# Kernel optimization log

Hardware: AMD Instinct MI355X
Metric: run time of the kernel (lower is better)

Reference implementation:

```python
import jax, jax.numpy as jnp
import numpy as np

N = 50000      # nodes
E = 800000     # edges (avg degree 16)
F_IN = 128     # num_node_features
H = 128        # hidden_dim
G = 500        # num graphs in batch


def setup_inputs() -> dict:
    key = jax.random.key(0)
    ks = jax.random.split(key, 20)
    inp = {
        "x": jax.random.normal(ks[0], (N, F_IN), dtype=jnp.float32),
        "edge_index": jax.random.randint(ks[1], (2, E), 0, N, dtype=jnp.int32),
        "batch": jnp.sort(jax.random.randint(ks[2], (N,), 0, G, dtype=jnp.int32)),
    }
    s = 0.05
    # 3 GIN layers: MLP = Linear -> ReLU -> Linear, plus learnable eps (init 0)
    dims = [(F_IN, H), (H, H), (H, H)]
    for i, (din, dout) in enumerate(dims):
        k = jax.random.split(ks[3 + i], 4)
        inp[f"W1_{i}"] = jax.random.normal(k[0], (din, H), dtype=jnp.float32) * s
        inp[f"b1_{i}"] = jnp.zeros((H,), dtype=jnp.float32)
        inp[f"W2_{i}"] = jax.random.normal(k[1], (H, dout), dtype=jnp.float32) * s
        inp[f"b2_{i}"] = jnp.zeros((dout,), dtype=jnp.float32)
        inp[f"eps_{i}"] = jnp.zeros((), dtype=jnp.float32)
    inp["fc_w"] = jax.random.normal(ks[10], (H, 1), dtype=jnp.float32) * s
    inp["fc_b"] = jnp.zeros((1,), dtype=jnp.float32)
    return inp


def _gin_layer(x, src, dst, eps, W1, b1, W2, b2):
    # neighbor sum: scatter-add messages x[src] into dst rows
    agg = jax.ops.segment_sum(x[src], dst, num_segments=N)  # [N, d]
    h = (1.0 + eps) * x + agg
    h = jax.nn.relu(h @ W1 + b1) @ W2 + b2
    return h


def reference(x, edge_index, batch,
              W1_0, b1_0, W2_0, b2_0, eps_0,
              W1_1, b1_1, W2_1, b2_1, eps_1,
              W1_2, b1_2, W2_2, b2_2, eps_2,
              fc_w, fc_b):
    src, dst = edge_index[0], edge_index[1]
    layers = [(eps_0, W1_0, b1_0, W2_0, b2_0),
              (eps_1, W1_1, b1_1, W2_1, b2_1),
              (eps_2, W1_2, b1_2, W2_2, b2_2)]
    h = x
    for i, (eps, W1, b1, W2, b2) in enumerate(layers):
        h = _gin_layer(h, src, dst, eps, W1, b1, W2, b2)
        if i < len(layers) - 1:
            h = jax.nn.relu(h)  # dropout is identity in eval mode
    # global mean pool over graph ids
    sums = jax.ops.segment_sum(h, batch, num_segments=G)          # [G, H]
    counts = jax.ops.segment_sum(jnp.ones((N,), h.dtype), batch, num_segments=G)
    pooled = sums / jnp.maximum(counts, 1.0)[:, None]
    out = pooled @ fc_w + fc_b  # [G, 1]
    return jnp.squeeze(out, axis=-1)  # [G]
```

## Files before the change

kernel.cpp:

```cpp
#include <hip/hip_runtime.h>


#define FEAT 128
#define BCAP 2048
#define CHUNK 10240

typedef short  bf16x8 __attribute__((ext_vector_type(8)));
typedef float  f32x4  __attribute__((ext_vector_type(4)));

__device__ inline unsigned short f2bf(float f) {
    unsigned int u = __float_as_uint(f);
    u = (u + 0x7FFFu + ((u >> 16) & 1u)) >> 16;
    return (unsigned short)u;
}
__device__ inline float2 bfpair(unsigned int u) {
    float2 r;
    r.x = __uint_as_float(u << 16);
    r.y = __uint_as_float(u & 0xffff0000u);
    return r;
}

__global__ __launch_bounds__(1024) void bucket_kernel(
    const int* __restrict__ src, const int* __restrict__ dst,
    int* __restrict__ bcnt, unsigned int* __restrict__ bpairs, int E) {
    __shared__ unsigned int lpairs[CHUNK];
    __shared__ int lbase[1025];
    __shared__ int lcur[1024];
    __shared__ int lres[1024];
    __shared__ int part[1024];
    int tid = threadIdx.x;
    int e0 = blockIdx.x * CHUNK;
    int e1 = e0 + CHUNK; if (e1 > E) e1 = E;
    int cnt = e1 - e0;
    lcur[tid] = 0;
    __syncthreads();
    for (int e = e0 + tid; e < e1; e += 1024) atomicAdd(&lcur[dst[e] >> 6], 1);
    __syncthreads();
    int v = lcur[tid];
    part[tid] = v;
    __syncthreads();
    for (int d = 1; d < 1024; d <<= 1) {
        int u = (tid >= d) ? part[tid - d] : 0;
        __syncthreads();
        part[tid] += u;
        __syncthreads();
    }
    int ex = part[tid] - v;
    lbase[tid] = ex;
    if (tid == 1023) lbase[1024] = part[1023];
    lcur[tid] = ex;
    lres[tid] = (v > 0) ? atomicAdd(&bcnt[tid * 16], v) : 0;
    __syncthreads();
    for (int e = e0 + tid; e < e1; e += 1024) {
        int d = dst[e], s = src[e];
        int p = atomicAdd(&lcur[d >> 6], 1);
        lpairs[p] = ((unsigned int)s << 6) | (unsigned int)(d & 63);
    }
    __syncthreads();
    for (int j = tid; j < cnt; j += 1024) {
        int lo = 0, hi = 1023;
        while (lo < hi) { int m = (lo + hi + 1) >> 1; if (lbase[m] <= j) lo = m; else hi = m - 1; }
        int gpos = lres[lo] + (j - lbase[lo]);
        if (gpos < BCAP) bpairs[(size_t)lo * BCAP + gpos] = lpairs[j];
    }
}

__global__ void scan_bcnt_kernel(const int* __restrict__ bcnt, int* __restrict__ bbase,
                                 int* __restrict__ off, int n, int nbuckets) {
    __shared__ int l[1024];
    int t = threadIdx.x;
    int v = (t < nbuckets) ? bcnt[t * 16] : 0;
    l[t] = v;
    __syncthreads();
    for (int d = 1; d < 1024; d <<= 1) {
        int u = (t >= d) ? l[t - d] : 0;
        __syncthreads();
        l[t] += u;
        __syncthreads();
    }
    if (t < nbuckets) bbase[t] = l[t] - v;
    if (t == 1023) off[n] = l[1023];
}

__global__ __launch_bounds__(256) void degscat_kernel(
    const int* __restrict__ bcnt, const int* __restrict__ bbase,
    const unsigned int* __restrict__ bpairs,
    int* __restrict__ off, int* __restrict__ srcs, int n) {
    __shared__ int lh[64];
    __shared__ int lcur[64];
    int b = blockIdx.x, tid = threadIdx.x;
    if (tid < 64) lh[tid] = 0;
    __syncthreads();
    int cnt = bcnt[b * 16]; if (cnt > BCAP) cnt = BCAP;
    int base = bbase[b];
    const unsigned int* bp = bpairs + (size_t)b * BCAP;
    for (int i = tid; i < cnt; i += 256) atomicAdd(&lh[bp[i] & 63u], 1);
    __syncthreads();
    if (tid < 64) {
        int v = lh[tid];
        int inc = v;
        #pragma unroll
        for (int d = 1; d < 64; d <<= 1) {
            int u = __shfl_up(inc, d, 64);
            if (tid >= d) inc += u;
        }
        int ex = base + inc - v;
        int node = b * 64 + tid;
        if (node < n) off[node] = ex;
        lcur[tid] = ex;
    }
    __syncthreads();
    for (int i = tid; i < cnt; i += 256) {
        unsigned int pr = bp[i];
        int pos = atomicAdd(&lcur[pr & 63u], 1);
        srcs[pos] = (int)(pr >> 6);
    }
}

__global__ __launch_bounds__(256) void setup_kernel(
    const float* __restrict__ x, unsigned int* __restrict__ xbf, long pairs, int nxb,
    const int* __restrict__ batch, int* __restrict__ gstart, int n, int G,
    const float* __restrict__ W2f, const float* __restrict__ b2f,
    const float* __restrict__ fcw, float* __restrict__ weff,
    const float* __restrict__ W0, const float* __restrict__ W1,
    const float* __restrict__ W2, const float* __restrict__ W3,
    const float* __restrict__ W4, unsigned short* __restrict__ Wswz) {
    int b = blockIdx.x, tid = threadIdx.x;
    if (b < nxb) {
        long i = (long)b * 256 + tid;
        if (i < pairs) {
            float2 v = ((const float2*)x)[i];
            unsigned int pk = (unsigned int)f2bf(v.x) | ((unsigned int)f2bf(v.y) << 16);
            long node = i >> 6;
            int dg = (int)(i & 63);
            int slice = dg >> 4, d = dg & 15;
            xbf[(size_t)slice * n * 16 + node * 16 + d] = pk;
        }
    } else if (b < nxb + 2) {
        int i = (b - nxb) * 256 + tid;
        if (i <= G) {
            int lo = 0, hi = n;
            while (lo < hi) { int m = (lo + hi) >> 1; if (batch[m] < i) lo = m + 1; else hi = m; }
            gstart[i] = lo;
        }
    } else if (b == nxb + 2) {
        int lane = tid & 63, wave = tid >> 6;
        float2 f2 = ((const float2*)fcw)[lane];
        for (int r = wave; r < 128; r += 4) {
            float2 w = ((const float2*)(W2f + r * FEAT))[lane];
            float d = w.x * f2.x + w.y * f2.y;
            #pragma unroll
            for (int s = 32; s; s >>= 1) d += __shfl_down(d, s, 64);
            if (lane == 0) weff[r] = d;
        }
        if (wave == 0) {
            float2 bb = ((const float2*)b2f)[lane];
            float d = bb.x * f2.x + bb.y * f2.y;
            #pragma unroll
            for (int s = 32; s; s >>= 1) d += __shfl_down(d, s, 64);
            if (lane == 0) weff[128] = d;
        }
    } else {
        int gid = (b - nxb - 3) * 256 + tid;
        if (gid < 5 * 2048) {
            int mat = gid >> 11;
            int task = gid & 2047;
            int c = task >> 4, m = task & 15;
            const float* W = (mat == 0) ? W0 : (mat == 1) ? W1 : (mat == 2) ? W2 :
                             (mat == 3) ? W3 : W4;
            unsigned short* dp = Wswz + mat * 16384 + c * 128 + ((m ^ (c & 7)) << 3);
            #pragma unroll
            for (int j = 0; j < 8; ++j) dp[j] = f2bf(W[(8 * m + j) * FEAT + c]);
        }
    }
}

__global__ __launch_bounds__(256) void agg_kernel(
    const unsigned int* __restrict__ hs, const int* __restrict__ off,
    const int* __restrict__ srcs, const float* __restrict__ eps_p,
    unsigned int* __restrict__ pre, int n) {
    int b = blockIdx.x;
    int slice = b & 3;
    int chunk = b >> 2;
    int tid = threadIdx.x;
    int wave = tid >> 6, lane = tid & 63;
    int g = lane >> 2, d = lane & 3;
    int node = chunk * 64 + wave * 16 + g;
    if (node >= n) return;
    float eps1 = 1.0f + eps_p[0];
    const uint4* hb = (const uint4*)(hs + (size_t)slice * n * 16);
    uint4 su = hb[(size_t)node * 4 + d];
    float2 p0 = bfpair(su.x), p1 = bfpair(su.y), p2 = bfpair(su.z), p3 = bfpair(su.w);
    float4 a0 = make_float4(p0.x * eps1, p0.y * eps1, p1.x * eps1, p1.y * eps1);
    float4 b0 = make_float4(p2.x * eps1, p2.y * eps1, p3.x * eps1, p3.y * eps1);
    float4 a1 = make_float4(0.f, 0.f, 0.f, 0.f), b1v = a1;
    float4 a2 = a1, b2v = a1;
    float4 a3 = a1, b3v = a1;
    int j0 = off[node], j1 = off[node + 1];
    int j = j0;
    #define ACC(A, B, U) { float2 q0 = bfpair(U.x), q1 = bfpair(U.y), \
                                  q2 = bfpair(U.z), q3 = bfpair(U.w); \
        A.x += q0.x; A.y += q0.y; A.z += q1.x; A.w += q1.y; \
        B.x += q2.x; B.y += q2.y; B.z += q3.x; B.w += q3.y; }
    for (; j + 8 <= j1; j += 8) {
        int s0 = srcs[j], s1 = srcs[j + 1], s2 = srcs[j + 2], s3 = srcs[j + 3];
        int s4 = srcs[j + 4], s5 = srcs[j + 5], s6 = srcs[j + 6], s7 = srcs[j + 7];
        uint4 u0 = hb[(size_t)s0 * 4 + d];
        uint4 u1 = hb[(size_t)s1 * 4 + d];
        uint4 u2 = hb[(size_t)s2 * 4 + d];
        uint4 u3 = hb[(size_t)s3 * 4 + d];
        uint4 u4 = hb[(size_t)s4 * 4 + d];
        uint4 u5 = hb[(size_t)s5 * 4 + d];
        uint4 u6 = hb[(size_t)s6 * 4 + d];
        uint4 u7 = hb[(size_t)s7 * 4 + d];
        ACC(a0, b0, u0) ACC(a1, b1v, u1) ACC(a2, b2v, u2) ACC(a3, b3v, u3)
        ACC(a0, b0, u4) ACC(a1, b1v, u5) ACC(a2, b2v, u6) ACC(a3, b3v, u7)
    }
    for (; j + 4 <= j1; j += 4) {
        int s0 = srcs[j], s1 = srcs[j + 1], s2 = srcs[j + 2], s3 = srcs[j + 3];
        uint4 u0 = hb[(size_t)s0 * 4 + d];
        uint4 u1 = hb[(size_t)s1 * 4 + d];
        uint4 u2 = hb[(size_t)s2 * 4 + d];
        uint4 u3 = hb[(size_t)s3 * 4 + d];
        ACC(a0, b0, u0) ACC(a1, b1v, u1) ACC(a2, b2v, u2) ACC(a3, b3v, u3)
    }
    for (; j < j1; ++j) {
        uint4 u = hb[(size_t)srcs[j] * 4 + d];
        ACC(a0, b0, u)
    }
    #undef ACC
    a0.x += a1.x + a2.x;  a0.y += a1.y + a2.y;
    a0.z += a1.z + a2.z;  a0.w += a1.w + a2.w;
    a0.x += a3.x;  a0.y += a3.y;  a0.z += a3.z;  a0.w += a3.w;
    b0.x += b1v.x + b2v.x;  b0.y += b1v.y + b2v.y;
    b0.z += b1v.z + b2v.z;  b0.w += b1v.w + b2v.w;
    b0.x += b3v.x;  b0.y += b3v.y;  b0.z += b3v.z;  b0.w += b3v.w;
    uint4 o;
    o.x = (unsigned int)f2bf(a0.x) | ((unsigned int)f2bf(a0.y) << 16);
    o.y = (unsigned int)f2bf(a0.z) | ((unsigned int)f2bf(a0.w) << 16);
    o.z = (unsigned int)f2bf(b0.x) | ((unsigned int)f2bf(b0.y) << 16);
    o.w = (unsigned int)f2bf(b0.z) | ((unsigned int)f2bf(b0.w) << 16);
    ((uint4*)(pre + (size_t)slice * n * 16))[(size_t)node * 4 + d] = o;
}

template <int MODE>
__global__ __launch_bounds__(256) void mfma_mlp_kernel(
    const unsigned short* __restrict__ A, const unsigned short* __restrict__ Wswz,
    const float* __restrict__ bias, unsigned short* __restrict__ outbf,
    const int* __restrict__ batch, const float* __restrict__ weff,
    float* __restrict__ sums, int n) {
    __shared__ int4 Wl4[2048];
    int tid = threadIdx.x;
    const int4* ws4 = (const int4*)Wswz;
    #pragma unroll
    for (int i = 0; i < 8; ++i) Wl4[i * 256 + tid] = ws4[i * 256 + tid];
    __syncthreads();
    const unsigned short* Wl = (const unsigned short*)Wl4;

    int lane = tid & 63, wave = tid >> 6;
    int q = lane >> 4, c15 = lane & 15;
    int r0 = blockIdx.x * 64 + wave * 16;
    int arow = r0 + c15;
    bool rv = arow < n;
    size_t sstride = (size_t)n * 32;
    const unsigned short* abase = A + (size_t)arow * 32 + 8 * q;

    f32x4 zf = {0.f, 0.f, 0.f, 0.f};
    f32x4 acc[8];
    #pragma unroll
    for (int i = 0; i < 8; ++i) acc[i] = zf;
    bf16x8 zero8 = {0, 0, 0, 0, 0, 0, 0, 0};

    #pragma unroll
    for (int k0 = 0; k0 < 4; ++k0) {
        bf16x8 a = rv ? *(const bf16x8*)(abase + (size_t)k0 * sstride) : zero8;
        int m = k0 * 4 + q;
        #pragma unroll
        for (int nt = 0; nt < 8; ++nt) {
            int col = nt * 16 + c15;
            bf16x8 bfr = *(const bf16x8*)&Wl[col * 128 + ((m ^ (col & 7)) << 3)];
            acc[nt] = __builtin_amdgcn_mfma_f32_16x16x32_bf16(a, bfr, acc[nt], 0, 0, 0);
        }
    }

    int orow0 = r0 + q * 4;
    if (MODE == 1) {
        #pragma unroll
        for (int nt = 0; nt < 8; ++nt) {
            float bv = bias[nt * 16 + c15];
            size_t sb = (size_t)(nt >> 1) * sstride + (nt & 1) * 16 + c15;
            #pragma unroll
            for (int r = 0; r < 4; ++r) {
                int ro = orow0 + r;
                if (ro < n) {
                    float v = fmaxf(acc[nt][r] + bv, 0.f);
                    outbf[sb + (size_t)ro * 32] = f2bf(v);
                }
            }
        }
    } else {
        __shared__ float gsum[64];
        int r0b = blockIdx.x * 64;
        int lastn = r0b + 63 < n - 1 ? r0b + 63 : n - 1;
        int gmin = batch[r0b];
        int gmax = batch[lastn];
        int span = gmax - gmin + 1;
        bool lds_ok = (span <= 64);
        if (lds_ok) for (int i = tid; i < span; i += 256) gsum[i] = 0.f;
        __syncthreads();
        float rowdot[4] = {0.f, 0.f, 0.f, 0.f};
        #pragma unroll
        for (int nt = 0; nt < 8; ++nt) {
            int col = nt * 16 + c15;
            float bv = bias[col];
            float wv = weff[col];
            #pragma unroll
            for (int r = 0; r < 4; ++r)
                rowdot[r] += fmaxf(acc[nt][r] + bv, 0.f) * wv;
        }
        #pragma unroll
        for (int r = 0; r < 4; ++r) {
            float v = rowdot[r];
            v += __shfl_xor(v, 1, 64);
            v += __shfl_xor(v, 2, 64);
            v += __shfl_xor(v, 4, 64);
            v += __shfl_xor(v, 8, 64);
            if (c15 == 0) {
                int node = orow0 + r;
                if (node < n) {
                    int g = batch[node];
                    if (lds_ok) atomicAdd(&gsum[g - gmin], v);
                    else        atomicAdd(&sums[g], v);
                }
            }
        }
        __syncthreads();
        if (lds_ok)
            for (int i = tid; i < span; i += 256) atomicAdd(&sums[gmin + i], gsum[i]);
    }
}

__global__ void finalize_kernel(const float* __restrict__ sums, const int* __restrict__ gstart,
                                const float* __restrict__ weff, const float* __restrict__ fcb,
                                float* __restrict__ out, int G) {
    int g = blockIdx.x * blockDim.x + threadIdx.x;
    if (g >= G) return;
    int cnt = gstart[g + 1] - gstart[g];
    out[g] = (cnt > 0) ? sums[g] / (float)cnt + weff[128] + fcb[0] : fcb[0];
}

static inline size_t align256(size_t x) { return (x + 255) & ~(size_t)255; }

extern "C" void kernel_launch(void* const* d_in, const int* in_sizes, int n_in,
                              void* d_out, int out_size, void* d_ws, size_t ws_size,
                              hipStream_t stream) {
    const float* x      = (const float*)d_in[0];
    const int*   ei     = (const int*)d_in[1];
    const int*   batch  = (const int*)d_in[2];
    const float* W1[3]  = {(const float*)d_in[3],  (const float*)d_in[8],  (const float*)d_in[13]};
    const float* b1[3]  = {(const float*)d_in[4],  (const float*)d_in[9],  (const float*)d_in[14]};
    const float* W2[3]  = {(const float*)d_in[5],  (const float*)d_in[10], (const float*)d_in[15]};
    const float* b2[3]  = {(const float*)d_in[6],  (const float*)d_in[11], (const float*)d_in[16]};
    const float* eps[3] = {(const float*)d_in[7],  (const float*)d_in[12], (const float*)d_in[17]};
    const float* fcw    = (const float*)d_in[18];
    const float* fcb    = (const float*)d_in[19];
    float* out = (float*)d_out;

    const int N = in_sizes[0] / FEAT;
    const int E = in_sizes[1] / 2;
    const int G = out_size;
    const int nbuckets = (N + 63) >> 6;

    char* p = (char*)d_ws;
    int* off    = (int*)p;  p += align256((size_t)(N + 1) * 4);
    int* srcs   = (int*)p;  p += align256((size_t)E * 4);
    int* bbase  = (int*)p;  p += align256((size_t)1024 * 4);
    int* gstart = (int*)p;  p += align256((size_t)(G + 1) * 4);
    float* weff = (float*)p; p += align256((size_t)256 * 4);
    unsigned short* Wswz = (unsigned short*)p; p += align256((size_t)5 * 16384 * 2);
    float* sums = (float*)p;
    char* z0 = (char*)sums;
    p += align256((size_t)G * 4);
    int* bcnt = (int*)p; p += align256((size_t)nbuckets * 16 * 4);
    size_t zbytes = (size_t)(p - z0);
    unsigned int* bpairs = (unsigned int*)p;     p += align256((size_t)nbuckets * BCAP * 4);
    unsigned int* x_bf   = (unsigned int*)p;     p += align256((size_t)N * 64 * 4);
    unsigned int* pre_bf = (unsigned int*)p;     p += align256((size_t)N * 64 * 4);
    unsigned int* t_bf   = (unsigned int*)p;     p += align256((size_t)N * 64 * 4);
    unsigned int* h_bf   = (unsigned int*)p;     p += align256((size_t)N * 64 * 4);
    (void)ws_size; (void)n_in;

    const int* src = ei;
    const int* dst = ei + E;

    hipMemsetAsync(z0, 0, zbytes, stream);

    const int nchunks = (E + CHUNK - 1) / CHUNK;
    bucket_kernel<<<nchunks, 1024, 0, stream>>>(src, dst, bcnt, bpairs, E);
    scan_bcnt_kernel<<<1, 1024, 0, stream>>>(bcnt, bbase, off, N, nbuckets);
    degscat_kernel<<<nbuckets, 256, 0, stream>>>(bcnt, bbase, bpairs, off, srcs, N);

    long pairs = (long)N * 64;
    int nxb = (int)((pairs + 255) / 256);
    setup_kernel<<<nxb + 43, 256, 0, stream>>>(
        x, x_bf, pairs, nxb, batch, gstart, N, G,
        W2[2], b2[2], fcw, weff,
        W1[0], W2[0], W1[1], W2[1], W1[2], Wswz);

    const int aggBlocks  = 4 * ((N + 63) / 64);
    const int gemmBlocks = (N + 63) / 64;
    const unsigned short* Wz[5] = {Wswz, Wswz + 16384, Wswz + 2 * 16384,
                                   Wswz + 3 * 16384, Wswz + 4 * 16384};

    const unsigned int* h = x_bf;
    for (int i = 0; i < 2; ++i) {
        agg_kernel<<<aggBlocks, 256, 0, stream>>>(h, off, srcs, eps[i], pre_bf, N);
        mfma_mlp_kernel<1><<<gemmBlocks, 256, 0, stream>>>(
            (const unsigned short*)pre_bf, Wz[2 * i], b1[i], (unsigned short*)t_bf,
            nullptr, nullptr, nullptr, N);
        mfma_mlp_kernel<1><<<gemmBlocks, 256, 0, stream>>>(
            (const unsigned short*)t_bf, Wz[2 * i + 1], b2[i], (unsigned short*)h_bf,
            nullptr, nullptr, nullptr, N);
        h = h_bf;
    }
    agg_kernel<<<aggBlocks, 256, 0, stream>>>(h, off, srcs, eps[2], pre_bf, N);
    mfma_mlp_kernel<2><<<gemmBlocks, 256, 0, stream>>>(
        (const unsigned short*)pre_bf, Wz[4], b1[2], nullptr,
        batch, weff, sums, N);

    finalize_kernel<<<(G + 255) / 256, 256, 0, stream>>>(sums, gstart, weff, fcb, out, G);
}
```

Baseline: 295.5 us.

## Merge setup kernels, drop bucket scan kernel, fold finalize into last GEMM

Bucketing and the setup work (bf16 conversion, graph starts, weight swizzle, folded fc weights) now run as one 1024-thread launch. The separate bucket-count scan kernel is removed: each degscat block sums the preceding bucket counts itself, and off[n] is set to E directly. The finalize kernel is replaced by a last-block-done pattern inside the final MLP kernel, using an atomic counter and a thread fence. The aim is to cut three launches and their gaps, at the cost of redundant prefix sums in degscat, larger blocks for the conversion work, and off[n]=E being wrong if any bucket overflows BCAP.

```diff
diff --git a/kernel.cpp b/kernel.cpp
--- a/kernel.cpp
+++ b/kernel.cpp
@@ -20,114 +20,63 @@
     return r;
 }
 
-__global__ __launch_bounds__(1024) void bucket_kernel(
+__global__ __launch_bounds__(1024) void front_kernel(
     const int* __restrict__ src, const int* __restrict__ dst,
-    int* __restrict__ bcnt, unsigned int* __restrict__ bpairs, int E) {
-    __shared__ unsigned int lpairs[CHUNK];
-    __shared__ int lbase[1025];
-    __shared__ int lcur[1024];
-    __shared__ int lres[1024];
-    __shared__ int part[1024];
-    int tid = threadIdx.x;
-    int e0 = blockIdx.x * CHUNK;
-    int e1 = e0 + CHUNK; if (e1 > E) e1 = E;
-    int cnt = e1 - e0;
-    lcur[tid] = 0;
-    __syncthreads();
-    for (int e = e0 + tid; e < e1; e += 1024) atomicAdd(&lcur[dst[e] >> 6], 1);
-    __syncthreads();
-    int v = lcur[tid];
-    part[tid] = v;
-    __syncthreads();
-    for (int d = 1; d < 1024; d <<= 1) {
-        int u = (tid >= d) ? part[tid - d] : 0;
-        __syncthreads();
-        part[tid] += u;
-        __syncthreads();
-    }
-    int ex = part[tid] - v;
-    lbase[tid] = ex;
-    if (tid == 1023) lbase[1024] = part[1023];
-    lcur[tid] = ex;
-    lres[tid] = (v > 0) ? atomicAdd(&bcnt[tid * 16], v) : 0;
-    __syncthreads();
-    for (int e = e0 + tid; e < e1; e += 1024) {
-        int d = dst[e], s = src[e];
-        int p = atomicAdd(&lcur[d >> 6], 1);
-        lpairs[p] = ((unsigned int)s << 6) | (unsigned int)(d & 63);
-    }
-    __syncthreads();
-    for (int j = tid; j < cnt; j += 1024) {
-        int lo = 0, hi = 1023;
-        while (lo < hi) { int m = (lo + hi + 1) >> 1; if (lbase[m] <= j) lo = m; else hi = m - 1; }
-        int gpos = lres[lo] + (j - lbase[lo]);
-        if (gpos < BCAP) bpairs[(size_t)lo * BCAP + gpos] = lpairs[j];
-    }
-}
-
-__global__ void scan_bcnt_kernel(const int* __restrict__ bcnt, int* __restrict__ bbase,
-                                 int* __restrict__ off, int n, int nbuckets) {
-    __shared__ int l[1024];
-    int t = threadIdx.x;
-    int v = (t < nbuckets) ? bcnt[t * 16] : 0;
-    l[t] = v;
-    __syncthreads();
-    for (int d = 1; d < 1024; d <<= 1) {
-        int u = (t >= d) ? l[t - d] : 0;
-        __syncthreads();
-        l[t] += u;
-        __syncthreads();
-    }
-    if (t < nbuckets) bbase[t] = l[t] - v;
-    if (t == 1023) off[n] = l[1023];
-}
-
-__global__ __launch_bounds__(256) void degscat_kernel(
-    const int* __restrict__ bcnt, const int* __restrict__ bbase,
-    const unsigned int* __restrict__ bpairs,
-    int* __restrict__ off, int* __restrict__ srcs, int n) {
-    __shared__ int lh[64];
-    __shared__ int lcur[64];
-    int b = blockIdx.x, tid = threadIdx.x;
-    if (tid < 64) lh[tid] = 0;
-    __syncthreads();
-    int cnt = bcnt[b * 16]; if (cnt > BCAP) cnt = BCAP;
-    int base = bbase[b];
-    const unsigned int* bp = bpairs + (size_t)b * BCAP;
-    for (int i = tid; i < cnt; i += 256) atomicAdd(&lh[bp[i] & 63u], 1);
-    __syncthreads();
-    if (tid < 64) {
-        int v = lh[tid];
-        int inc = v;
-        #pragma unroll
-        for (int d = 1; d < 64; d <<= 1) {
-            int u = __shfl_up(inc, d, 64);
-            if (tid >= d) inc += u;
-        }
-        int ex = base + inc - v;
-        int node = b * 64 + tid;
-        if (node < n) off[node] = ex;
-        lcur[tid] = ex;
-    }
-    __syncthreads();
-    for (int i = tid; i < cnt; i += 256) {
-        unsigned int pr = bp[i];
-        int pos = atomicAdd(&lcur[pr & 63u], 1);
-        srcs[pos] = (int)(pr >> 6);
-    }
-}
-
-__global__ __launch_bounds__(256) void setup_kernel(
-    const float* __restrict__ x, unsigned int* __restrict__ xbf, long pairs, int nxb,
+    int* __restrict__ bcnt, unsigned int* __restrict__ bpairs, int E, int nchunks,
+    const float* __restrict__ x, unsigned int* __restrict__ xbf, long pairs, int nxbf,
     const int* __restrict__ batch, int* __restrict__ gstart, int n, int G,
     const float* __restrict__ W2f, const float* __restrict__ b2f,
     const float* __restrict__ fcw, float* __restrict__ weff,
     const float* __restrict__ W0, const float* __restrict__ W1,
     const float* __restrict__ W2, const float* __restrict__ W3,
     const float* __restrict__ W4, unsigned short* __restrict__ Wswz) {
+    __shared__ unsigned int lpairs[CHUNK];
+    __shared__ int lbase[1025];
+    __shared__ int lcur[1024];
+    __shared__ int lres[1024];
+    __shared__ int part[1024];
     int b = blockIdx.x, tid = threadIdx.x;
-    if (b < nxb) {
-        long i = (long)b * 256 + tid;
+
+    if (b < nchunks) {
+        int e0 = b * CHUNK;
+        int e1 = e0 + CHUNK; if (e1 > E) e1 = E;
+        int cnt = e1 - e0;
+        lcur[tid] = 0;
+        __syncthreads();
+        for (int e = e0 + tid; e < e1; e += 1024) atomicAdd(&lcur[dst[e] >> 6], 1);
+        __syncthreads();
+        int v = lcur[tid];
+        part[tid] = v;
+        __syncthreads();
+        for (int d = 1; d < 1024; d <<= 1) {
+            int u = (tid >= d) ? part[tid - d] : 0;
+            __syncthreads();
+            part[tid] += u;
+            __syncthreads();
+        }
+        int ex = part[tid] - v;
+        lbase[tid] = ex;
+        if (tid == 1023) lbase[1024] = part[1023];
+        lcur[tid] = ex;
+        lres[tid] = (v > 0) ? atomicAdd(&bcnt[tid * 16], v) : 0;
+        __syncthreads();
+        for (int e = e0 + tid; e < e1; e += 1024) {
+            int d = dst[e], s = src[e];
+            int p = atomicAdd(&lcur[d >> 6], 1);
+            lpairs[p] = ((unsigned int)s << 6) | (unsigned int)(d & 63);
+        }
+        __syncthreads();
+        for (int j = tid; j < cnt; j += 1024) {
+            int lo = 0, hi = 1023;
+            while (lo < hi) { int m = (lo + hi + 1) >> 1; if (lbase[m] <= j) lo = m; else hi = m - 1; }
+            int gpos = lres[lo] + (j - lbase[lo]);
+            if (gpos < BCAP) bpairs[(size_t)lo * BCAP + gpos] = lpairs[j];
+        }
+        return;
+    }
+    b -= nchunks;
+    if (b < nxbf) {
+        long i = (long)b * 1024 + tid;
         if (i < pairs) {
             float2 v = ((const float2*)x)[i];
             unsigned int pk = (unsigned int)f2bf(v.x) | ((unsigned int)f2bf(v.y) << 16);
@@ -136,17 +85,21 @@
             int slice = dg >> 4, d = dg & 15;
             xbf[(size_t)slice * n * 16 + node * 16 + d] = pk;
         }
-    } else if (b < nxb + 2) {
-        int i = (b - nxb) * 256 + tid;
-        if (i <= G) {
+        return;
+    }
+    b -= nxbf;
+    if (b == 0) {
+        for (int i = tid; i <= G; i += 1024) {
             int lo = 0, hi = n;
             while (lo < hi) { int m = (lo + hi) >> 1; if (batch[m] < i) lo = m + 1; else hi = m; }
             gstart[i] = lo;
         }
-    } else if (b == nxb + 2) {
+        return;
+    }
+    if (b == 1) {
         int lane = tid & 63, wave = tid >> 6;
         float2 f2 = ((const float2*)fcw)[lane];
-        for (int r = wave; r < 128; r += 4) {
+        for (int r = wave; r < 128; r += 16) {
             float2 w = ((const float2*)(W2f + r * FEAT))[lane];
             float d = w.x * f2.x + w.y * f2.y;
             #pragma unroll
@@ -160,8 +113,10 @@
             for (int s = 32; s; s >>= 1) d += __shfl_down(d, s, 64);
             if (lane == 0) weff[128] = d;
         }
-    } else {
-        int gid = (b - nxb - 3) * 256 + tid;
+        return;
+    }
+    {
+        int gid = (b - 2) * 1024 + tid;
         if (gid < 5 * 2048) {
             int mat = gid >> 11;
             int task = gid & 2047;
@@ -172,6 +127,45 @@
             #pragma unroll
             for (int j = 0; j < 8; ++j) dp[j] = f2bf(W[(8 * m + j) * FEAT + c]);
         }
+    }
+}
+
+__global__ __launch_bounds__(256) void degscat_kernel(
+    const int* __restrict__ bcnt, const unsigned int* __restrict__ bpairs,
+    int* __restrict__ off, int* __restrict__ srcs, int n, int E) {
+    __shared__ int lh[64];
+    __shared__ int lcur[64];
+    int b = blockIdx.x, tid = threadIdx.x;
+    if (tid < 64) lh[tid] = 0;
+    if (b == 0 && tid == 0) off[n] = E;
+    __syncthreads();
+    int cnt = bcnt[b * 16]; if (cnt > BCAP) cnt = BCAP;
+    const unsigned int* bp = bpairs + (size_t)b * BCAP;
+    for (int i = tid; i < cnt; i += 256) atomicAdd(&lh[bp[i] & 63u], 1);
+    __syncthreads();
+    if (tid < 64) {
+        int bp_ = 0;
+        for (int k = tid; k < b; k += 64) bp_ += bcnt[k * 16];
+        #pragma unroll
+        for (int d = 32; d; d >>= 1) bp_ += __shfl_down(bp_, d, 64);
+        int base = __shfl(bp_, 0, 64);
+        int v = lh[tid];
+        int inc = v;
+        #pragma unroll
+        for (int d = 1; d < 64; d <<= 1) {
+            int u = __shfl_up(inc, d, 64);
+            if (tid >= d) inc += u;
+        }
+        int ex = base + inc - v;
+        int node = b * 64 + tid;
+        if (node < n) off[node] = ex;
+        lcur[tid] = ex;
+    }
+    __syncthreads();
+    for (int i = tid; i < cnt; i += 256) {
+        unsigned int pr = bp[i];
+        int pos = atomicAdd(&lcur[pr & 63u], 1);
+        srcs[pos] = (int)(pr >> 6);
     }
 }
 
@@ -248,7 +242,9 @@
     const unsigned short* __restrict__ A, const unsigned short* __restrict__ Wswz,
     const float* __restrict__ bias, unsigned short* __restrict__ outbf,
     const int* __restrict__ batch, const float* __restrict__ weff,
-    float* __restrict__ sums, int n) {
+    float* __restrict__ sums, int* __restrict__ donecnt,
+    const int* __restrict__ gstart, const float* __restrict__ fcb,
+    float* __restrict__ out, int G, int n) {
     __shared__ int4 Wl4[2048];
     int tid = threadIdx.x;
     const int4* ws4 = (const int4*)Wswz;
@@ -300,6 +296,7 @@
         }
     } else {
         __shared__ float gsum[64];
+        __shared__ int amlast;
         int r0b = blockIdx.x * 64;
         int lastn = r0b + 63 < n - 1 ? r0b + 63 : n - 1;
         int gmin = batch[r0b];
@@ -337,16 +334,18 @@
         __syncthreads();
         if (lds_ok)
             for (int i = tid; i < span; i += 256) atomicAdd(&sums[gmin + i], gsum[i]);
-    }
-}
-
-__global__ void finalize_kernel(const float* __restrict__ sums, const int* __restrict__ gstart,
-                                const float* __restrict__ weff, const float* __restrict__ fcb,
-                                float* __restrict__ out, int G) {
-    int g = blockIdx.x * blockDim.x + threadIdx.x;
-    if (g >= G) return;
-    int cnt = gstart[g + 1] - gstart[g];
-    out[g] = (cnt > 0) ? sums[g] / (float)cnt + weff[128] + fcb[0] : fcb[0];
+        __threadfence();
+        __syncthreads();
+        if (tid == 0) amlast = (atomicAdd(donecnt, 1) == (int)gridDim.x - 1) ? 1 : 0;
+        __syncthreads();
+        if (amlast) {
+            for (int g = tid; g < G; g += 256) {
+                int cg = gstart[g + 1] - gstart[g];
+                float sv = ((volatile float*)sums)[g];
+                out[g] = (cg > 0) ? sv / (float)cg + weff[128] + fcb[0] : fcb[0];
+            }
+        }
+    }
 }
 
 static inline size_t align256(size_t x) { return (x + 255) & ~(size_t)255; }
@@ -374,13 +373,13 @@
     char* p = (char*)d_ws;
     int* off    = (int*)p;  p += align256((size_t)(N + 1) * 4);
     int* srcs   = (int*)p;  p += align256((size_t)E * 4);
-    int* bbase  = (int*)p;  p += align256((size_t)1024 * 4);
     int* gstart = (int*)p;  p += align256((size_t)(G + 1) * 4);
     float* weff = (float*)p; p += align256((size_t)256 * 4);
     unsigned short* Wswz = (unsigned short*)p; p += align256((size_t)5 * 16384 * 2);
     float* sums = (float*)p;
     char* z0 = (char*)sums;
     p += align256((size_t)G * 4);
+    int* donecnt = (int*)p; p += align256(256);
     int* bcnt = (int*)p; p += align256((size_t)nbuckets * 16 * 4);
     size_t zbytes = (size_t)(p - z0);
     unsigned int* bpairs = (unsigned int*)p;     p += align256((size_t)nbuckets * BCAP * 4);
@@ -396,16 +395,15 @@
     hipMemsetAsync(z0, 0, zbytes, stream);
 
     const int nchunks = (E + CHUNK - 1) / CHUNK;
-    bucket_kernel<<<nchunks, 1024, 0, stream>>>(src, dst, bcnt, bpairs, E);
-    scan_bcnt_kernel<<<1, 1024, 0, stream>>>(bcnt, bbase, off, N, nbuckets);
-    degscat_kernel<<<nbuckets, 256, 0, stream>>>(bcnt, bbase, bpairs, off, srcs, N);
-
     long pairs = (long)N * 64;
-    int nxb = (int)((pairs + 255) / 256);
-    setup_kernel<<<nxb + 43, 256, 0, stream>>>(
-        x, x_bf, pairs, nxb, batch, gstart, N, G,
+    int nxbf = (int)((pairs + 1023) / 1024);
+    front_kernel<<<nchunks + nxbf + 2 + 10, 1024, 0, stream>>>(
+        src, dst, bcnt, bpairs, E, nchunks,
+        x, x_bf, pairs, nxbf, batch, gstart, N, G,
         W2[2], b2[2], fcw, weff,
         W1[0], W2[0], W1[1], W2[1], W1[2], Wswz);
+
+    degscat_kernel<<<nbuckets, 256, 0, stream>>>(bcnt, bpairs, off, srcs, N, E);
 
     const int aggBlocks  = 4 * ((N + 63) / 64);
     const int gemmBlocks = (N + 63) / 64;
@@ -417,16 +415,14 @@
         agg_kernel<<<aggBlocks, 256, 0, stream>>>(h, off, srcs, eps[i], pre_bf, N);
         mfma_mlp_kernel<1><<<gemmBlocks, 256, 0, stream>>>(
             (const unsigned short*)pre_bf, Wz[2 * i], b1[i], (unsigned short*)t_bf,
-            nullptr, nullptr, nullptr, N);
+            nullptr, nullptr, nullptr, nullptr, nullptr, nullptr, nullptr, 0, N);
         mfma_mlp_kernel<1><<<gemmBlocks, 256, 0, stream>>>(
             (const unsigned short*)t_bf, Wz[2 * i + 1], b2[i], (unsigned short*)h_bf,
-            nullptr, nullptr, nullptr, N);
+            nullptr, nullptr, nullptr, nullptr, nullptr, nullptr, nullptr, 0, N);
         h = h_bf;
     }
     agg_kernel<<<aggBlocks, 256, 0, stream>>>(h, off, srcs, eps[2], pre_bf, N);
     mfma_mlp_kernel<2><<<gemmBlocks, 256, 0, stream>>>(
         (const unsigned short*)pre_bf, Wz[4], b1[2], nullptr,
-        batch, weff, sums, N);
-
-    finalize_kernel<<<(G + 255) / 256, 256, 0, stream>>>(sums, gstart, weff, fcb, out, G);
-}
+        batch, weff, sums, donecnt, gstart, fcb, out, G, N);
+}
```

Measured after the change: 316.8 us. 7.2% more time.
